# Performance work log

Hardware: AMD Instinct MI355X
Metric: run time of the kernel (lower is better)

Reference implementation:

```python
import jax, jax.numpy as jnp
import numpy as np
from jax.scipy.special import logsumexp

T, B, H, K = 256, 256, 512, 64


def setup_inputs() -> dict:
    key = jax.random.key(0)
    k1, k2, k3, k4, k5, k6, k7, k8 = jax.random.split(key, 8)
    hiddens = jax.random.normal(k1, (T, B, H), dtype=jnp.float32)
    lens = jax.random.randint(k2, (B,), 1, T + 1)              # sentence lengths in [1, T]
    tags = jax.random.randint(k3, (T, B), 0, K)                # gold tags
    W = jax.random.normal(k4, (K, H), dtype=jnp.float32) * (1.0 / np.sqrt(H))
    b = jax.random.normal(k5, (K,), dtype=jnp.float32) * 0.01
    begin_transition = jax.random.normal(k6, (K,), dtype=jnp.float32)
    transition = jax.random.normal(k7, (K, K), dtype=jnp.float32)
    end_transition = jax.random.normal(k8, (K,), dtype=jnp.float32)
    return {"hiddens": hiddens, "lens": lens, "tags": tags, "W": W, "b": b,
            "begin_transition": begin_transition, "transition": transition,
            "end_transition": end_transition}


def reference(hiddens, lens, tags, W, b, begin_transition, transition, end_transition):
    # emissions: [T, B, K] = hidden2emission(hiddens)
    em = jnp.einsum('tbh,kh->tbk', hiddens, W) + b
    t_len, batch, k = em.shape

    # ---- forward (partition) score: log-semiring DP over time ----
    alpha0 = em[0] + begin_transition                       # [B, K]

    def step(alpha, e_t):
        # alpha_t[b, j] = logsumexp_i(alpha[b, i] + transition[j, i]) + e_t[b, j]
        a = logsumexp(alpha[:, None, :] + transition[None, :, :], axis=-1) + e_t
        return a, a

    _, alphas = jax.lax.scan(step, alpha0, em[1:])          # [T-1, B, K]
    alphas = jnp.concatenate([alpha0[None], alphas], axis=0)  # [T, B, K]

    bidx = jnp.arange(batch)
    last_alpha = alphas[lens - 1, bidx]                     # [B, K] at each sentence end
    forward_score = logsumexp(last_alpha + end_transition, axis=-1)  # [B]

    # ---- gold path score ----
    em_g = jnp.take_along_axis(em, tags[:, :, None], axis=-1)[..., 0]   # [T, B]
    inc = transition[tags[1:], tags[:-1]] + em_g[1:]                     # [T-1, B]
    first = (begin_transition[tags[0]] + em_g[0])[None]                  # [1, B]
    scores = jnp.cumsum(jnp.concatenate([first, inc], axis=0), axis=0)   # [T, B]
    last_scores = scores[lens - 1, bidx]                                 # [B]
    last_tags = tags[lens - 1, bidx]
    gold_score = last_scores + end_transition[last_tags]                 # [B]

    return jnp.sum(forward_score - gold_score)
```

## Files before the change

### kernel.cpp

```cpp
#include <hip/hip_runtime.h>
#include <hip/hip_bf16.h>
#include <math.h>

#define T_DIM 256
#define B_DIM 256
#define H_DIM 512
#define K_DIM 64
#define LN2F 0.69314718055994531f

typedef __attribute__((ext_vector_type(8))) short bfrag_t;
typedef __attribute__((ext_vector_type(4))) float f4_t;

__device__ inline bfrag_t pack8(float4 a, float4 b) {
  union { bfrag_t v; __hip_bfloat162 h[4]; } u;
  u.h[0] = __float22bfloat162_rn(float2{a.x, a.y});
  u.h[1] = __float22bfloat162_rn(float2{a.z, a.w});
  u.h[2] = __float22bfloat162_rn(float2{b.x, b.y});
  u.h[3] = __float22bfloat162_rn(float2{b.z, b.w});
  return u.v;
}

__device__ inline void async_ld16(const float* g, float* l) {
  __builtin_amdgcn_global_load_lds(
      (const __attribute__((address_space(1))) void*)g,
      (__attribute__((address_space(3))) void*)l, 16, 0, 0);
}

__global__ __launch_bounds__(256) void emis_gemm3(
    const float* __restrict__ hid,
    const float* __restrict__ W,
    const float* __restrict__ bias,
    float* __restrict__ emP)
{
  __shared__ float As[2][128 * 64];
  const int tid  = threadIdx.x;
  const int wv   = tid >> 6;
  const int lane = tid & 63;
  const int l16  = lane & 15;
  const int quad = lane >> 4;
  const int m0   = blockIdx.x * 128;

  bfrag_t bw[16];
  {
    const float* wr = W + (size_t)(wv * 16 + l16) * H_DIM + quad * 8;
#pragma unroll
    for (int kc = 0; kc < 16; ++kc)
      bw[kc] = pack8(*(const float4*)(wr + kc * 32), *(const float4*)(wr + kc * 32 + 4));
  }

  const int srow   = wv * 32 + (lane >> 4);
  const int schunk = (lane & 15) ^ ((lane >> 4) & 3);

  f4_t acc[8];
#pragma unroll
  for (int mt = 0; mt < 8; ++mt) acc[mt] = (f4_t){0.f, 0.f, 0.f, 0.f};

#pragma unroll
  for (int inst = 0; inst < 8; ++inst)
    async_ld16(hid + (size_t)(m0 + srow + inst * 4) * H_DIM + 0 * 64 + schunk * 4,
               &As[0][(wv * 32 + inst * 4) * 64]);
  __syncthreads();

  int buf = 0;
  for (int it = 0; it < 8; ++it) {
    if (it < 7) {
#pragma unroll
      for (int inst = 0; inst < 8; ++inst)
        async_ld16(hid + (size_t)(m0 + srow + inst * 4) * H_DIM + (it + 1) * 64 + schunk * 4,
                   &As[buf ^ 1][(wv * 32 + inst * 4) * 64]);
    }
#pragma unroll
    for (int kc2 = 0; kc2 < 2; ++kc2) {
#pragma unroll
      for (int mt = 0; mt < 8; ++mt) {
        const int row = mt * 16 + l16;
        const int c0  = (kc2 * 8 + quad * 2 + 0) ^ (l16 & 3);
        const int c1  = (kc2 * 8 + quad * 2 + 1) ^ (l16 & 3);
        const float4 a0 = *(const float4*)(&As[buf][row * 64 + c0 * 4]);
        const float4 a1 = *(const float4*)(&As[buf][row * 64 + c1 * 4]);
        acc[mt] = __builtin_amdgcn_mfma_f32_16x16x32_bf16(pack8(a0, a1), bw[it * 2 + kc2],
                                                          acc[mt], 0, 0, 0);
      }
    }
    __syncthreads();
    buf ^= 1;
  }

  const float bn = bias[wv * 16 + l16];
#pragma unroll
  for (int mt = 0; mt < 8; ++mt) {
#pragma unroll
    for (int r = 0; r < 4; ++r) {
      const int m = m0 + mt * 16 + quad * 4 + r;
      const int t = m >> 8;
      const int b = m & 255;
      const float v = __expf(acc[mt][r] + bn);
      emP[((((size_t)(b >> 4) * 256 + t) * 64 + (l16 >> 2) * 16 + (b & 15)) << 4)
          + wv * 4 + (l16 & 3)] = v;
    }
  }
}

__global__ __launch_bounds__(128) void crf_dp4(
    const float* __restrict__ emP,
    const int* __restrict__ lens,
    const int* __restrict__ tags,
    const float* __restrict__ trans,
    const float* __restrict__ beginT,
    const float* __restrict__ endT,
    float* __restrict__ out)
{
  const int g    = blockIdx.x;
  const int tid  = threadIdx.x;
  const int wv   = tid >> 6;
  const int lane = tid & 63;
  const int n    = lane & 15;
  const int q    = lane >> 4;
  const int b    = g * 16 + n;

  __shared__ float xs[64 * 16];
  __shared__ int   Lxs[64];
  __shared__ float s0d[16];
  __shared__ int   Ls0[16];
  __shared__ float gpart;

  const int len = lens[b];
  const int cap = len - 1;
  const float* base = emP + (((size_t)g * 256) * 64 + lane) * 16;

  float eend[16];
#pragma unroll
  for (int k = 0; k < 16; ++k)
    eend[k] = __expf(endT[(k >> 2) * 16 + q * 4 + (k & 3)]);

  float y[16];
  int Lint = 0;
  bfrag_t bf0, bf1;
  float wA[16], wB[16], wC[16], wD[16];
  float g0 = 0.f;

#define LOADW(dst, t) { \
    const float4 _a = *(const float4*)(base + (size_t)(t) * 1024 + 0); \
    const float4 _b = *(const float4*)(base + (size_t)(t) * 1024 + 4); \
    const float4 _c = *(const float4*)(base + (size_t)(t) * 1024 + 8); \
    const float4 _d = *(const float4*)(base + (size_t)(t) * 1024 + 12); \
    dst[0]=_a.x; dst[1]=_a.y; dst[2]=_a.z; dst[3]=_a.w; \
    dst[4]=_b.x; dst[5]=_b.y; dst[6]=_b.z; dst[7]=_b.w; \
    dst[8]=_c.x; dst[9]=_c.y; dst[10]=_c.z; dst[11]=_c.w; \
    dst[12]=_d.x; dst[13]=_d.y; dst[14]=_d.z; dst[15]=_d.w; }

#define RESCALE() { \
    float _mx = y[0]; \
    _Pragma("unroll") for (int k = 1; k < 16; ++k) _mx = fmaxf(_mx, y[k]); \
    _mx = fmaxf(_mx, __shfl_xor(_mx, 16)); \
    _mx = fmaxf(_mx, __shfl_xor(_mx, 32)); \
    int _e; (void)frexpf(_mx, &_e); \
    Lint += _e; \
    _Pragma("unroll") for (int k = 0; k < 16; ++k) y[k] = ldexpf(y[k], -_e); }

#define BUILDBV(S) { \
    union { bfrag_t v; __hip_bfloat162 h[4]; } _u0, _u1; \
    _u0.h[0] = __float22bfloat162_rn(float2{S[0], S[1]}); \
    _u0.h[1] = __float22bfloat162_rn(float2{S[2], S[3]}); \
    _u0.h[2] = __float22bfloat162_rn(float2{S[4], S[5]}); \
    _u0.h[3] = __float22bfloat162_rn(float2{S[6], S[7]}); \
    _u1.h[0] = __float22bfloat162_rn(float2{S[8], S[9]}); \
    _u1.h[1] = __float22bfloat162_rn(float2{S[10], S[11]}); \
    _u1.h[2] = __float22bfloat162_rn(float2{S[12], S[13]}); \
    _u1.h[3] = __float22bfloat162_rn(float2{S[14], S[15]}); \
    bf0 = _u0.v; bf1 = _u1.v; }

  const f4_t zro = (f4_t){0.f, 0.f, 0.f, 0.f};

#define EMPIDX(tt, tg) (((((size_t)g * 256 + (tt)) * 64 + (((tg) >> 2) & 3) * 16 + n) << 4) \
                        + ((tg) >> 4) * 4 + ((tg) & 3))

  if (wv == 0) {
    bfrag_t aE[8];
#pragma unroll
    for (int jt = 0; jt < 4; ++jt)
#pragma unroll
      for (int kt = 0; kt < 2; ++kt) {
        union { bfrag_t v; __hip_bfloat16 h[8]; } u;
#pragma unroll
        for (int r = 0; r < 8; ++r) {
          const int i = (2 * kt + (r >> 2)) * 16 + q * 4 + (r & 3);
          u.h[r] = __float2bfloat16(__expf(trans[(jt * 16 + n) * K_DIM + i]));
        }
        aE[jt * 2 + kt] = u.v;
      }

    float snap[16];
    int Lsnap = 0;
    LOADW(wA, 0);
#pragma unroll
    for (int k = 0; k < 16; ++k) {
      const int j = (k >> 2) * 16 + q * 4 + (k & 3);
      y[k] = wA[k] * __expf(beginT[j]);
      snap[k] = (cap == 0) ? y[k] : 0.0f;
    }
    RESCALE(); BUILDBV(y);
    LOADW(wA, 1); LOADW(wB, 2); LOADW(wC, 3); LOADW(wD, 4);

#define STEPF(T, W, RSC) { \
    f4_t _a0 = __builtin_amdgcn_mfma_f32_16x16x32_bf16(aE[0], bf0, zro, 0, 0, 0); \
    f4_t _a1 = __builtin_amdgcn_mfma_f32_16x16x32_bf16(aE[2], bf0, zro, 0, 0, 0); \
    f4_t _a2 = __builtin_amdgcn_mfma_f32_16x16x32_bf16(aE[4], bf0, zro, 0, 0, 0); \
    f4_t _a3 = __builtin_amdgcn_mfma_f32_16x16x32_bf16(aE[6], bf0, zro, 0, 0, 0); \
    _a0 = __builtin_amdgcn_mfma_f32_16x16x32_bf16(aE[1], bf1, _a0, 0, 0, 0); \
    _a1 = __builtin_amdgcn_mfma_f32_16x16x32_bf16(aE[3], bf1, _a1, 0, 0, 0); \
    _a2 = __builtin_amdgcn_mfma_f32_16x16x32_bf16(aE[5], bf1, _a2, 0, 0, 0); \
    _a3 = __builtin_amdgcn_mfma_f32_16x16x32_bf16(aE[7], bf1, _a3, 0, 0, 0); \
    _Pragma("unroll") for (int r = 0; r < 4; ++r) { \
      y[r]      = _a0[r] * W[r]; \
      y[4 + r]  = _a1[r] * W[4 + r]; \
      y[8 + r]  = _a2[r] * W[8 + r]; \
      y[12 + r] = _a3[r] * W[12 + r]; } \
    const bool _hit = ((T) == cap); \
    _Pragma("unroll") for (int k = 0; k < 16; ++k) snap[k] = _hit ? y[k] : snap[k]; \
    Lsnap = _hit ? Lint : Lsnap; \
    if (RSC) { RESCALE(); } \
    BUILDBV(y); }

    int t = 1;
    for (int it = 0; it < 31; ++it, t += 4) {
      STEPF(t, wA, 0);     LOADW(wA, t + 4);
      STEPF(t + 1, wB, 0); LOADW(wB, t + 5);
      STEPF(t + 2, wC, 0); LOADW(wC, t + 6);
      STEPF(t + 3, wD, 1); LOADW(wD, t + 7);
    }
    STEPF(125, wA, 0); STEPF(126, wB, 0); STEPF(127, wC, 0);

#pragma unroll
    for (int k = 0; k < 16; ++k) xs[lane * 16 + k] = y[k];
    Lxs[lane] = Lint;
    float sd = 0.f;
#pragma unroll
    for (int k = 0; k < 16; ++k) sd += snap[k] * eend[k];
    sd += __shfl_xor(sd, 16);
    sd += __shfl_xor(sd, 32);
    if (lane < 16) { s0d[lane] = sd; Ls0[lane] = Lsnap; }

    for (int c = 0; c < 32; ++c) {
      const int tt = q + 4 * c;
      if (tt < len) {
        const int tg = tags[(size_t)tt * B_DIM + b];
        float v = __logf(emP[EMPIDX(tt, tg)]);
        v += (tt == 0) ? beginT[tg]
                       : trans[(size_t)tg * K_DIM + tags[(size_t)(tt - 1) * B_DIM + b]];
        if (tt == cap) v += endT[tg];
        g0 += v;
      }
    }
    float gr = g0;
#pragma unroll
    for (int o = 1; o < 64; o <<= 1) gr += __shfl_xor(gr, o);
    if (lane == 0) gpart = gr;
  } else {
    bfrag_t aET[8];
#pragma unroll
    for (int jt = 0; jt < 4; ++jt)
#pragma unroll
      for (int kt = 0; kt < 2; ++kt) {
        union { bfrag_t v; __hip_bfloat16 h[8]; } u;
#pragma unroll
        for (int r = 0; r < 8; ++r) {
          const int i = (2 * kt + (r >> 2)) * 16 + q * 4 + (r & 3);
          u.h[r] = __float2bfloat16(__expf(trans[(size_t)i * K_DIM + (jt * 16 + n)]));
        }
        aET[jt * 2 + kt] = u.v;
      }

#pragma unroll
    for (int k = 0; k < 16; ++k) y[k] = 0.f;
    LOADW(wA, 255); LOADW(wB, 254); LOADW(wC, 253); LOADW(wD, 252);

#define STEPB(T, W, RSC) { \
    const bool _hit = ((T) == cap); \
    float _d[16]; \
    _Pragma("unroll") for (int k = 0; k < 16; ++k) \
      _d[k] = (_hit ? eend[k] : y[k]) * W[k]; \
    BUILDBV(_d); \
    f4_t _a0 = __builtin_amdgcn_mfma_f32_16x16x32_bf16(aET[0], bf0, zro, 0, 0, 0); \
    f4_t _a1 = __builtin_amdgcn_mfma_f32_16x16x32_bf16(aET[2], bf0, zro, 0, 0, 0); \
    f4_t _a2 = __builtin_amdgcn_mfma_f32_16x16x32_bf16(aET[4], bf0, zro, 0, 0, 0); \
    f4_t _a3 = __builtin_amdgcn_mfma_f32_16x16x32_bf16(aET[6], bf0, zro, 0, 0, 0); \
    _a0 = __builtin_amdgcn_mfma_f32_16x16x32_bf16(aET[1], bf1, _a0, 0, 0, 0); \
    _a1 = __builtin_amdgcn_mfma_f32_16x16x32_bf16(aET[3], bf1, _a1, 0, 0, 0); \
    _a2 = __builtin_amdgcn_mfma_f32_16x16x32_bf16(aET[5], bf1, _a2, 0, 0, 0); \
    _a3 = __builtin_amdgcn_mfma_f32_16x16x32_bf16(aET[7], bf1, _a3, 0, 0, 0); \
    _Pragma("unroll") for (int r = 0; r < 4; ++r) { \
      y[r]      = _a0[r]; \
      y[4 + r]  = _a1[r]; \
      y[8 + r]  = _a2[r]; \
      y[12 + r] = _a3[r]; } \
    if (RSC) { RESCALE(); } }

    int t = 255;
    for (int it = 0; it < 32; ++it, t -= 4) {
      STEPB(t, wA, 0);     LOADW(wA, t - 4);
      STEPB(t - 1, wB, 0); LOADW(wB, t - 5);
      STEPB(t - 2, wC, 0); LOADW(wC, t - 6);
      STEPB(t - 3, wD, 1); LOADW(wD, t - 7);
    }

    for (int c = 0; c < 32; ++c) {
      const int tt = 128 + q + 4 * c;
      if (tt < len) {
        const int tg = tags[(size_t)tt * B_DIM + b];
        float v = __logf(emP[EMPIDX(tt, tg)]);
        v += trans[(size_t)tg * K_DIM + tags[(size_t)(tt - 1) * B_DIM + b]];
        if (tt == cap) v += endT[tg];
        g0 += v;
      }
    }
  }

  __syncthreads();

  if (wv == 1) {
    float dot1 = 0.f;
#pragma unroll
    for (int k = 0; k < 16; ++k) dot1 += xs[lane * 16 + k] * y[k];
    dot1 += __shfl_xor(dot1, 16);
    dot1 += __shfl_xor(dot1, 32);

    const bool hi = (cap >= 128);
    const float dsel = hi ? dot1 : s0d[n];
    const float Lsel = (float)(hi ? (Lxs[lane] + Lint) : Ls0[n]);
    const float f = __logf(dsel) + Lsel * LN2F;

    float r = 0.25f * f - g0;
#pragma unroll
    for (int o = 1; o < 64; o <<= 1) r += __shfl_xor(r, o);
    if (lane == 0) atomicAdd(out, r - gpart);
  }
}

extern "C" void kernel_launch(void* const* d_in, const int* in_sizes, int n_in,
                              void* d_out, int out_size, void* d_ws, size_t ws_size,
                              hipStream_t stream) {
  const float* hiddens = (const float*)d_in[0];
  const int*   lens    = (const int*)  d_in[1];
  const int*   tags    = (const int*)  d_in[2];
  const float* W       = (const float*)d_in[3];
  const float* bias    = (const float*)d_in[4];
  const float* beginT  = (const float*)d_in[5];
  const float* trans   = (const float*)d_in[6];
  const float* endT    = (const float*)d_in[7];

  float* emP = (float*)d_ws;
  float* out = (float*)d_out;

  hipMemsetAsync(out, 0, sizeof(float), stream);
  emis_gemm3<<<(T_DIM * B_DIM) / 128, 256, 0, stream>>>(hiddens, W, bias, emP);
  crf_dp4<<<16, 128, 0, stream>>>(emP, lens, tags, trans, beginT, endT, out);
}
```

Measured before the change: 279.3 us.

## Rework emission GEMM staging and deepen DP prefetch pipeline

The emission GEMM now uses 64-row tiles. Each thread converts hiddens to bf16 in registers before storing to padded LDS, replacing async fp32 global-to-LDS loads. Results are staged through LDS so emP is written with coalesced float4 stores. The CRF DP kernel raises its register prefetch depth for emission tiles from four steps to eight and rescales every four steps instead of every four-step group end. This aims to hide global-load latency in the serial DP chain and improve GEMM occupancy and store coalescing. The cost is higher register pressure from the eight buffers.

```diff
diff --git a/kernel.cpp b/kernel.cpp
--- a/kernel.cpp
+++ b/kernel.cpp
@@ -20,25 +20,21 @@
   return u.v;
 }
 
-__device__ inline void async_ld16(const float* g, float* l) {
-  __builtin_amdgcn_global_load_lds(
-      (const __attribute__((address_space(1))) void*)g,
-      (__attribute__((address_space(3))) void*)l, 16, 0, 0);
-}
-
-__global__ __launch_bounds__(256) void emis_gemm3(
+__global__ __launch_bounds__(256, 3) void emis_gemm5(
     const float* __restrict__ hid,
     const float* __restrict__ W,
     const float* __restrict__ bias,
     float* __restrict__ emP)
 {
-  __shared__ float As[2][128 * 64];
+  __shared__ __hip_bfloat16 AsH[2][64 * 72];
+  float* Cs = (float*)&AsH[0][0];
+
   const int tid  = threadIdx.x;
   const int wv   = tid >> 6;
   const int lane = tid & 63;
   const int l16  = lane & 15;
   const int quad = lane >> 4;
-  const int m0   = blockIdx.x * 128;
+  const int m0   = blockIdx.x * 64;
 
   bfrag_t bw[16];
   {
@@ -48,60 +44,68 @@
       bw[kc] = pack8(*(const float4*)(wr + kc * 32), *(const float4*)(wr + kc * 32 + 4));
   }
 
-  const int srow   = wv * 32 + (lane >> 4);
-  const int schunk = (lane & 15) ^ ((lane >> 4) & 3);
-
-  f4_t acc[8];
-#pragma unroll
-  for (int mt = 0; mt < 8; ++mt) acc[mt] = (f4_t){0.f, 0.f, 0.f, 0.f};
-
-#pragma unroll
-  for (int inst = 0; inst < 8; ++inst)
-    async_ld16(hid + (size_t)(m0 + srow + inst * 4) * H_DIM + 0 * 64 + schunk * 4,
-               &As[0][(wv * 32 + inst * 4) * 64]);
+  const int sr = tid >> 2;
+  const int sc = (tid & 3) << 4;
+  const float* hrow = hid + (size_t)(m0 + sr) * H_DIM + sc;
+
+  f4_t acc[4];
+#pragma unroll
+  for (int mt = 0; mt < 4; ++mt) acc[mt] = (f4_t){0.f, 0.f, 0.f, 0.f};
+
+  float4 p0 = *(const float4*)(hrow + 0);
+  float4 p1 = *(const float4*)(hrow + 4);
+  float4 p2 = *(const float4*)(hrow + 8);
+  float4 p3 = *(const float4*)(hrow + 12);
+  *(bfrag_t*)(&AsH[0][sr * 72 + sc + 0]) = pack8(p0, p1);
+  *(bfrag_t*)(&AsH[0][sr * 72 + sc + 8]) = pack8(p2, p3);
   __syncthreads();
 
-  int buf = 0;
+#pragma unroll
   for (int it = 0; it < 8; ++it) {
     if (it < 7) {
-#pragma unroll
-      for (int inst = 0; inst < 8; ++inst)
-        async_ld16(hid + (size_t)(m0 + srow + inst * 4) * H_DIM + (it + 1) * 64 + schunk * 4,
-                   &As[buf ^ 1][(wv * 32 + inst * 4) * 64]);
+      p0 = *(const float4*)(hrow + (it + 1) * 64 + 0);
+      p1 = *(const float4*)(hrow + (it + 1) * 64 + 4);
+      p2 = *(const float4*)(hrow + (it + 1) * 64 + 8);
+      p3 = *(const float4*)(hrow + (it + 1) * 64 + 12);
     }
 #pragma unroll
     for (int kc2 = 0; kc2 < 2; ++kc2) {
 #pragma unroll
-      for (int mt = 0; mt < 8; ++mt) {
-        const int row = mt * 16 + l16;
-        const int c0  = (kc2 * 8 + quad * 2 + 0) ^ (l16 & 3);
-        const int c1  = (kc2 * 8 + quad * 2 + 1) ^ (l16 & 3);
-        const float4 a0 = *(const float4*)(&As[buf][row * 64 + c0 * 4]);
-        const float4 a1 = *(const float4*)(&As[buf][row * 64 + c1 * 4]);
-        acc[mt] = __builtin_amdgcn_mfma_f32_16x16x32_bf16(pack8(a0, a1), bw[it * 2 + kc2],
-                                                          acc[mt], 0, 0, 0);
-      }
+      for (int mt = 0; mt < 4; ++mt) {
+        const bfrag_t af =
+            *(const bfrag_t*)(&AsH[it & 1][(mt * 16 + l16) * 72 + kc2 * 32 + quad * 8]);
+        acc[mt] = __builtin_amdgcn_mfma_f32_16x16x32_bf16(af, bw[it * 2 + kc2], acc[mt], 0, 0, 0);
+      }
+    }
+    if (it < 7) {
+      *(bfrag_t*)(&AsH[(it + 1) & 1][sr * 72 + sc + 0]) = pack8(p0, p1);
+      *(bfrag_t*)(&AsH[(it + 1) & 1][sr * 72 + sc + 8]) = pack8(p2, p3);
     }
     __syncthreads();
-    buf ^= 1;
   }
 
   const float bn = bias[wv * 16 + l16];
 #pragma unroll
-  for (int mt = 0; mt < 8; ++mt) {
-#pragma unroll
-    for (int r = 0; r < 4; ++r) {
-      const int m = m0 + mt * 16 + quad * 4 + r;
-      const int t = m >> 8;
-      const int b = m & 255;
-      const float v = __expf(acc[mt][r] + bn);
-      emP[((((size_t)(b >> 4) * 256 + t) * 64 + (l16 >> 2) * 16 + (b & 15)) << 4)
-          + wv * 4 + (l16 & 3)] = v;
-    }
+  for (int mt = 0; mt < 4; ++mt)
+#pragma unroll
+    for (int r = 0; r < 4; ++r)
+      Cs[(mt * 16 + quad * 4 + r) * 68 + wv * 16 + l16] = __expf(acc[mt][r] + bn);
+  __syncthreads();
+
+  const int t  = m0 >> 8;
+  const int g0 = (m0 & 255) >> 4;
+  const int bl = tid & 15;
+  const int qq = (tid >> 4) & 3;
+  const int gl = tid >> 6;
+#pragma unroll
+  for (int i = 0; i < 4; ++i) {
+    const float4 v = *(const float4*)(&Cs[(gl * 16 + bl) * 68 + i * 16 + qq * 4]);
+    const size_t off = (((size_t)(g0 + gl) * 256 + t) * 64 + qq * 16 + bl) * 16 + i * 4;
+    *(float4*)(emP + off) = v;
   }
 }
 
-__global__ __launch_bounds__(128) void crf_dp4(
+__global__ __launch_bounds__(128) void crf_dp5(
     const float* __restrict__ emP,
     const int* __restrict__ lens,
     const int* __restrict__ tags,
@@ -136,7 +140,7 @@
   float y[16];
   int Lint = 0;
   bfrag_t bf0, bf1;
-  float wA[16], wB[16], wC[16], wD[16];
+  float wA[16], wB[16], wC[16], wD[16], wE[16], wF[16], wG[16], wH[16];
   float g0 = 0.f;
 
 #define LOADW(dst, t) { \
@@ -201,6 +205,7 @@
     }
     RESCALE(); BUILDBV(y);
     LOADW(wA, 1); LOADW(wB, 2); LOADW(wC, 3); LOADW(wD, 4);
+    LOADW(wE, 5); LOADW(wF, 6); LOADW(wG, 7); LOADW(wH, 8);
 
 #define STEPF(T, W, RSC) { \
     f4_t _a0 = __builtin_amdgcn_mfma_f32_16x16x32_bf16(aE[0], bf0, zro, 0, 0, 0); \
@@ -223,13 +228,18 @@
     BUILDBV(y); }
 
     int t = 1;
-    for (int it = 0; it < 31; ++it, t += 4) {
-      STEPF(t, wA, 0);     LOADW(wA, t + 4);
-      STEPF(t + 1, wB, 0); LOADW(wB, t + 5);
-      STEPF(t + 2, wC, 0); LOADW(wC, t + 6);
-      STEPF(t + 3, wD, 1); LOADW(wD, t + 7);
-    }
-    STEPF(125, wA, 0); STEPF(126, wB, 0); STEPF(127, wC, 0);
+    for (int it = 0; it < 15; ++it, t += 8) {
+      STEPF(t + 0, wA, 0); LOADW(wA, t + 8);
+      STEPF(t + 1, wB, 0); LOADW(wB, t + 9);
+      STEPF(t + 2, wC, 1); LOADW(wC, t + 10);
+      STEPF(t + 3, wD, 0); LOADW(wD, t + 11);
+      STEPF(t + 4, wE, 0); LOADW(wE, t + 12);
+      STEPF(t + 5, wF, 0); LOADW(wF, t + 13);
+      STEPF(t + 6, wG, 1); LOADW(wG, t + 14);
+      STEPF(t + 7, wH, 0); LOADW(wH, t + 15);
+    }
+    STEPF(121, wA, 0); STEPF(122, wB, 0); STEPF(123, wC, 1); STEPF(124, wD, 0);
+    STEPF(125, wE, 0); STEPF(126, wF, 0); STEPF(127, wG, 0);
 
 #pragma unroll
     for (int k = 0; k < 16; ++k) xs[lane * 16 + k] = y[k];
@@ -274,6 +284,7 @@
 #pragma unroll
     for (int k = 0; k < 16; ++k) y[k] = 0.f;
     LOADW(wA, 255); LOADW(wB, 254); LOADW(wC, 253); LOADW(wD, 252);
+    LOADW(wE, 251); LOADW(wF, 250); LOADW(wG, 249); LOADW(wH, 248);
 
 #define STEPB(T, W, RSC) { \
     const bool _hit = ((T) == cap); \
@@ -297,11 +308,15 @@
     if (RSC) { RESCALE(); } }
 
     int t = 255;
-    for (int it = 0; it < 32; ++it, t -= 4) {
-      STEPB(t, wA, 0);     LOADW(wA, t - 4);
-      STEPB(t - 1, wB, 0); LOADW(wB, t - 5);
-      STEPB(t - 2, wC, 0); LOADW(wC, t - 6);
-      STEPB(t - 3, wD, 1); LOADW(wD, t - 7);
+    for (int it = 0; it < 16; ++it, t -= 8) {
+      STEPB(t - 0, wA, 0); LOADW(wA, t - 8);
+      STEPB(t - 1, wB, 0); LOADW(wB, t - 9);
+      STEPB(t - 2, wC, 1); LOADW(wC, t - 10);
+      STEPB(t - 3, wD, 0); LOADW(wD, t - 11);
+      STEPB(t - 4, wE, 0); LOADW(wE, t - 12);
+      STEPB(t - 5, wF, 0); LOADW(wF, t - 13);
+      STEPB(t - 6, wG, 1); LOADW(wG, t - 14);
+      STEPB(t - 7, wH, 0); LOADW(wH, t - 15);
     }
 
     for (int c = 0; c < 32; ++c) {
@@ -353,6 +368,6 @@
   float* out = (float*)d_out;
 
   hipMemsetAsync(out, 0, sizeof(float), stream);
-  emis_gemm3<<<(T_DIM * B_DIM) / 128, 256, 0, stream>>>(hiddens, W, bias, emP);
-  crf_dp4<<<16, 128, 0, stream>>>(emP, lens, tags, trans, beginT, endT, out);
+  emis_gemm5<<<(T_DIM * B_DIM) / 64, 256, 0, stream>>>(hiddens, W, bias, emP);
+  crf_dp5<<<16, 128, 0, stream>>>(emP, lens, tags, trans, beginT, endT, out);
 }
```

Measured after the change: 275.6 us. Within noise of the previous version (-1.3%).
